# Kernel optimization log

Hardware: AMD Instinct MI355X
Metric: run time of the kernel (lower is better)

## Reference

```python
import jax, jax.numpy as jnp
from jax import lax
import numpy as np

T, B, I, U = 512, 64, 512, 512
FORGET_BIAS = 1.0  # matches forget_bias=1.0; cell_clip=None -> no clipping; no peephole


def setup_inputs() -> dict:
    key = jax.random.key(0)
    kx, kw = jax.random.split(key)
    x = jax.random.normal(kx, (T, B, I), dtype=jnp.float32)
    cs0 = jnp.zeros((B, U), dtype=jnp.float32)
    h0 = jnp.zeros((B, U), dtype=jnp.float32)
    # kernel [input_size + num_units, 4*num_units], bias [4*num_units] (zeros init as in build())
    w = jax.random.normal(kw, (I + U, 4 * U), dtype=jnp.float32) * 0.05
    b = jnp.zeros((4 * U,), dtype=jnp.float32)
    return {"x": x, "cs0": cs0, "h0": h0, "w": w, "b": b}


def reference(x, cs0, h0, w, b):
    """Fused BlockLSTM forward. Returns (h_seq [T,B,U], final_cs, final_h),
    mirroring LSTMBlockWrapper.call -> (outputs, (cell_state, output))."""

    def step(carry, x_t):
        cs_prev, h_prev = carry
        z = jnp.concatenate([x_t, h_prev], axis=-1) @ w + b  # [B, 4U]
        # TF BlockLSTM gate order: i, ci (cell input), f, o
        zi, zci, zf, zo = jnp.split(z, 4, axis=-1)
        i = jax.nn.sigmoid(zi)
        f = jax.nn.sigmoid(zf + FORGET_BIAS)
        ci = jnp.tanh(zci)
        cs = ci * i + cs_prev * f  # no cell_clip (cell_clip=-1)
        h = jnp.tanh(cs) * jax.nn.sigmoid(zo)
        return (cs, h), h

    (final_cs, final_h), h_seq = lax.scan(step, (cs0, h0), x)
    return h_seq, final_cs, final_h
```

## Files before the change

### kernel.cpp

```cpp
#include <hip/hip_runtime.h>


#define T_STEPS 512
#define NB 64
#define NU 512
#define NI 512
#define KTOT 1024
#define ZCOLS 2048
#define HSEQ_ELEMS (T_STEPS * NB * NU)
#define POISON64 0x7FC07FC07FC07FC0ull

typedef float    floatx4   __attribute__((ext_vector_type(4)));
typedef __bf16   bf16x8    __attribute__((ext_vector_type(8)));
typedef unsigned short ushortx8 __attribute__((ext_vector_type(8)));
typedef unsigned long long ull_t;

static __device__ __forceinline__ unsigned short f2bf(float f) {
  unsigned int u = __builtin_bit_cast(unsigned int, f);
  u += 0x7fffu + ((u >> 16) & 1u);
  return (unsigned short)(u >> 16);
}
static __device__ __forceinline__ float bf2f(unsigned short h) {
  unsigned int u = ((unsigned int)h) << 16;
  return __builtin_bit_cast(float, u);
}
static __device__ __forceinline__ float asf(unsigned int u) {
  return __builtin_bit_cast(float, u);
}
static __device__ __forceinline__ float sigmoidf_(float x) {
  return __builtin_amdgcn_rcpf(1.0f + __expf(-x));
}
static __device__ __forceinline__ float fast_tanhf(float x) {
  const float ax = fabsf(x);
  const float t = __expf(-2.0f * ax);
  const float r = (1.0f - t) * __builtin_amdgcn_rcpf(1.0f + t);
  return copysignf(r, x);
}
static __device__ __forceinline__ bf16x8 ldfrag(const unsigned short* p) {
  ushortx8 v = *reinterpret_cast<const ushortx8*>(p);
  return __builtin_bit_cast(bf16x8, v);
}
static __device__ __forceinline__ ull_t pack4bf(float a, float b, float c, float d) {
  return (ull_t)f2bf(a) | ((ull_t)f2bf(b) << 16) | ((ull_t)f2bf(c) << 32) |
         ((ull_t)f2bf(d) << 48);
}
static __device__ __forceinline__ bf16x8 mkfrag(ull_t lo, ull_t hi) {
  struct P { ull_t a, b; } s{lo, hi};
  return __builtin_bit_cast(bf16x8, s);
}

__global__ __launch_bounds__(256) void init_kernel(const float* __restrict__ h0,
                                                   unsigned short* __restrict__ hbf) {
  const int j = blockIdx.x * 256 + threadIdx.x;
  if (j < 524288) {
    ull_t* p = reinterpret_cast<ull_t*>(&hbf[32768 + (size_t)j * 32]);
#pragma unroll
    for (int r = 0; r < 8; ++r) p[r] = POISON64;
  } else {
    const int k = j - 524288;
#pragma unroll
    for (int p2 = 0; p2 < 2; ++p2) {
      const int i = k * 2 + p2;
      const int row = i >> 6, chunk = i & 63;
      const float* src = &h0[row * NU + chunk * 8];
      const ull_t lo = pack4bf(src[0], src[1], src[2], src[3]);
      const ull_t hi = pack4bf(src[4], src[5], src[6], src[7]);
      const size_t off = ((size_t)((row >> 5) * 64 + chunk) * 32 + (row & 31)) * 8;
      *reinterpret_cast<ull_t*>(&hbf[off]) = lo;
      *reinterpret_cast<ull_t*>(&hbf[off + 4]) = hi;
    }
  }
}

__global__ __launch_bounds__(256) void transpose_w_kernel(
    const float* __restrict__ w, unsigned short* __restrict__ wT) {
  __shared__ float tile[32][33];
  const int u0 = blockIdx.x * 32;
  const int k0 = blockIdx.y * 32;
  const int g = blockIdx.z;
  const int tx = threadIdx.x & 31, ty = threadIdx.x >> 5;
#pragma unroll
  for (int r = 0; r < 4; ++r) {
    const int k = ty + r * 8;
    tile[k][tx] = w[(size_t)(k0 + k) * ZCOLS + g * 512 + u0 + tx];
  }
  __syncthreads();
#pragma unroll
  for (int r = 0; r < 4; ++r) {
    const int u = ty + r * 8;
    wT[(size_t)((u0 + u) * 4 + g) * KTOT + k0 + tx] = f2bf(tile[tx][u]);
  }
}

__global__ __launch_bounds__(256) void gemm_zx_kernel(
    const float* __restrict__ x, const unsigned short* __restrict__ wT,
    const float* __restrict__ bias, unsigned short* __restrict__ zxp) {
  __shared__ __align__(16) unsigned short As[128][32];
  __shared__ __align__(16) unsigned short Bs[128][32];
  const int m0 = blockIdx.y * 128;
  const int n0 = blockIdx.x * 128;
  const int tid = threadIdx.x;
  const int wid = tid >> 6, lane = tid & 63;
  const int quad = lane >> 4, nl = lane & 15;
  const int wm = (wid & 1) * 64, wn = (wid >> 1) * 64;
  const int srow = tid >> 3;
  const int skk = (tid & 7) * 4;

  floatx4 acc[4][4] = {};

  for (int kt = 0; kt < 16; ++kt) {
    const int k0 = kt * 32;
    __syncthreads();
#pragma unroll
    for (int r = 0; r < 4; ++r) {
      const int row = r * 32 + srow;
      const float4 v =
          *reinterpret_cast<const float4*>(&x[(size_t)(m0 + row) * NI + k0 + skk]);
      *reinterpret_cast<ull_t*>(&As[row][skk]) = pack4bf(v.x, v.y, v.z, v.w);
      *reinterpret_cast<ull_t*>(&Bs[row][skk]) =
          *reinterpret_cast<const ull_t*>(&wT[(size_t)(n0 + row) * KTOT + k0 + skk]);
    }
    __syncthreads();
    bf16x8 af[4], bfr[4];
#pragma unroll
    for (int i = 0; i < 4; ++i) {
      af[i] = ldfrag(&As[wm + i * 16 + nl][quad * 8]);
      bfr[i] = ldfrag(&Bs[wn + i * 16 + nl][quad * 8]);
    }
#pragma unroll
    for (int i = 0; i < 4; ++i)
#pragma unroll
      for (int j = 0; j < 4; ++j)
        acc[i][j] =
            __builtin_amdgcn_mfma_f32_16x16x32_bf16(af[i], bfr[j], acc[i][j], 0, 0, 0);
  }

  float bv[4];
#pragma unroll
  for (int j = 0; j < 4; ++j) {
    const int colp = n0 + wn + j * 16 + nl;
    bv[j] = bias[(colp & 3) * 512 + (colp >> 2)];
  }
#pragma unroll
  for (int i = 0; i < 4; ++i) {
    const int browb = wm + i * 16 + quad * 4;
    const int t = (m0 + browb) >> 6;
    const int rt = (browb >> 5) & 1;
    const int hi = (browb & 31) >> 3;
    const int qb = (browb >> 2) & 1;
#pragma unroll
    for (int j = 0; j < 4; ++j) {
      const int colp = n0 + wn + j * 16 + nl;
      const int cbl = colp >> 5;
      const int lanep = (colp & 31) + 32 * qb;
      const ull_t packed =
          pack4bf(acc[i][j][0] + bv[j], acc[i][j][1] + bv[j],
                  acc[i][j][2] + bv[j], acc[i][j][3] + bv[j]);
      *reinterpret_cast<ull_t*>(
          &zxp[((((size_t)t * 64 + cbl) * 2 + rt) * 64 + lanep) * 16 + hi * 4]) = packed;
    }
  }
}

__global__ __launch_bounds__(64, 1) void lstm_rec_kernel(
    const unsigned short* __restrict__ zxp, const unsigned short* __restrict__ wT,
    const float* __restrict__ cs_init, float* __restrict__ out,
    unsigned short* __restrict__ hbf) {
  const int lane = threadIdx.x;
  const int bid = blockIdx.x;
  const int cb = bid >> 2;
  const int qr = bid & 3;
  const int l15 = lane & 15, lq = lane >> 4;
  const int u0 = cb * 8;
  const int rowg = qr * 16 + l15;
  const int rh = qr >> 1;
  const int r31 = (qr & 1) * 16 + l15;

  bf16x8 Bf[2][16];
#pragma unroll
  for (int cf = 0; cf < 2; ++cf)
#pragma unroll
    for (int kf = 0; kf < 16; ++kf)
      Bf[cf][kf] = ldfrag(
          &wT[(size_t)(cb * 32 + cf * 16 + l15) * KTOT + 512 + kf * 32 + lq * 8]);

  float csv[2];
  csv[0] = cs_init[rowg * NU + u0 + 2 * lq];
  csv[1] = cs_init[rowg * NU + u0 + 2 * lq + 1];

  __shared__ float zsh[2][16][33];

  ull_t AL[16], AH[16];
  const unsigned short* hpbase =
      hbf + (size_t)rh * 16384 + (size_t)r31 * 8;

  auto issueA = [&](int t) {
    const unsigned short* hp = hpbase + (size_t)t * 32768 + lq * 256;
#pragma unroll
    for (int kf = 0; kf < 16; ++kf) {
      const unsigned short* p = hp + kf * 1024;
      AL[kf] = __hip_atomic_load((const ull_t*)p, __ATOMIC_RELAXED,
                                 __HIP_MEMORY_SCOPE_AGENT);
      AH[kf] = __hip_atomic_load((const ull_t*)(p + 4), __ATOMIC_RELAXED,
                                 __HIP_MEMORY_SCOPE_AGENT);
    }
  };

  const int hi4 = (qr & 1) * 2 + (lq >> 1);
  const int lanep_base = l15 + 32 * (lq & 1);
  ull_t zx0, zx1;
  auto issueZ = [&](int t) {
    const size_t base = ((((size_t)t * 64 + cb) * 2 + rh) * 64);
    zx0 = *reinterpret_cast<const ull_t*>(
        &zxp[(base + lanep_base) * 16 + 4 * hi4]);
    zx1 = *reinterpret_cast<const ull_t*>(
        &zxp[(base + lanep_base + 16) * 16 + 4 * hi4]);
  };

  issueA(0);
  issueZ(0);

  for (int t = 0; t < T_STEPS; ++t) {
    {
      int guard = 0;
      while (true) {
        float sx = 0.f, sy = 0.f, sz = 0.f, sw = 0.f;
#pragma unroll
        for (int kf = 0; kf < 16; ++kf) {
          sx += asf((unsigned)(AL[kf] & 0xffffffffu));
          sy += asf((unsigned)(AL[kf] >> 32));
          sz += asf((unsigned)(AH[kf] & 0xffffffffu));
          sw += asf((unsigned)(AH[kf] >> 32));
        }
        const float c = (sx + sy) + (sz + sw);
        if (!__any(c != c) || ++guard >= (1 << 18)) break;
        issueA(t);
      }
    }

    floatx4 a00, a01;
#pragma unroll
    for (int r = 0; r < 4; ++r) {
      a00[r] = bf2f((unsigned short)((zx0 >> (16 * r)) & 0xffffu));
      a01[r] = bf2f((unsigned short)((zx1 >> (16 * r)) & 0xffffu));
    }
    floatx4 a10 = {0.f, 0.f, 0.f, 0.f}, a11 = {0.f, 0.f, 0.f, 0.f};
#pragma unroll
    for (int kf = 0; kf < 8; ++kf) {
      const bf16x8 Alo = mkfrag(AL[kf], AH[kf]);
      const bf16x8 Ahi = mkfrag(AL[8 + kf], AH[8 + kf]);
      a00 = __builtin_amdgcn_mfma_f32_16x16x32_bf16(Alo, Bf[0][kf], a00, 0, 0, 0);
      a01 = __builtin_amdgcn_mfma_f32_16x16x32_bf16(Alo, Bf[1][kf], a01, 0, 0, 0);
      a10 = __builtin_amdgcn_mfma_f32_16x16x32_bf16(Ahi, Bf[0][8 + kf], a10, 0, 0, 0);
      a11 = __builtin_amdgcn_mfma_f32_16x16x32_bf16(Ahi, Bf[1][8 + kf], a11, 0, 0, 0);
    }
    const floatx4 zc0 = a00 + a10;
    const floatx4 zc1 = a01 + a11;

    const int pb = t & 1;
#pragma unroll
    for (int r = 0; r < 4; ++r) {
      zsh[pb][lq * 4 + r][l15] = zc0[r];
      zsh[pb][lq * 4 + r][16 + l15] = zc1[r];
    }
    const float4 g0 = *reinterpret_cast<const float4*>(&zsh[pb][l15][8 * lq]);
    const float4 g1 = *reinterpret_cast<const float4*>(&zsh[pb][l15][8 * lq + 4]);

    float hout[2];
    {
      const float iv = sigmoidf_(g0.x);
      const float civ = fast_tanhf(g0.y);
      const float fv = sigmoidf_(g0.z + 1.0f);
      const float ov = sigmoidf_(g0.w);
      csv[0] = civ * iv + csv[0] * fv;
      hout[0] = fast_tanhf(csv[0]) * ov;
    }
    {
      const float iv = sigmoidf_(g1.x);
      const float civ = fast_tanhf(g1.y);
      const float fv = sigmoidf_(g1.z + 1.0f);
      const float ov = sigmoidf_(g1.w);
      csv[1] = civ * iv + csv[1] * fv;
      hout[1] = fast_tanhf(csv[1]) * ov;
    }

    unsigned short* hw = &hbf[(size_t)(t + 1) * 32768 + (size_t)rh * 16384 +
                              cb * 256 + r31 * 8 + 2 * lq];
    const unsigned hv = (unsigned)f2bf(hout[0]) | ((unsigned)f2bf(hout[1]) << 16);
    __hip_atomic_store(reinterpret_cast<unsigned*>(hw), hv, __ATOMIC_RELAXED,
                       __HIP_MEMORY_SCOPE_AGENT);
    asm volatile("" ::: "memory");
    if (t + 1 < T_STEPS) {
      issueA(t + 1);
      issueZ(t + 1);
    }

    float* op = &out[((size_t)t * NB + rowg) * NU + u0 + 2 * lq];
    op[0] = hout[0];
    op[1] = hout[1];
    if (t == T_STEPS - 1) {
      float* cp = &out[HSEQ_ELEMS + (size_t)rowg * NU + u0 + 2 * lq];
      cp[0] = csv[0];
      cp[1] = csv[1];
      float* hp2 = &out[HSEQ_ELEMS + NB * NU + (size_t)rowg * NU + u0 + 2 * lq];
      hp2[0] = hout[0];
      hp2[1] = hout[1];
    }
  }
}

extern "C" void kernel_launch(void* const* d_in, const int* in_sizes, int n_in,
                              void* d_out, int out_size, void* d_ws, size_t ws_size,
                              hipStream_t stream) {
  const float* x = (const float*)d_in[0];
  const float* cs0 = (const float*)d_in[1];
  const float* h0 = (const float*)d_in[2];
  const float* w = (const float*)d_in[3];
  const float* bias = (const float*)d_in[4];
  float* out = (float*)d_out;

  char* ws = (char*)d_ws;
  unsigned short* wT = (unsigned short*)(ws);
  unsigned short* zxp = (unsigned short*)(ws + (size_t)(4 << 20));
  unsigned short* hbf = (unsigned short*)(ws + (size_t)(132 << 20));

  init_kernel<<<dim3(2056), 256, 0, stream>>>(h0, hbf);
  transpose_w_kernel<<<dim3(16, 32, 4), 256, 0, stream>>>(w, wT);
  gemm_zx_kernel<<<dim3(16, 256), 256, 0, stream>>>(x, wT, bias, zxp);
  lstm_rec_kernel<<<dim3(256), 64, 0, stream>>>(zxp, wT, cs0, out, hbf);
}
```

Baseline: 1.308 ms.

## Repartition recurrent LSTM kernel to 512 blocks with transposed MFMA and new h layout

Result: slower. 1.944 ms (+48.6%).

```diff
diff --git a/kernel.cpp b/kernel.cpp
--- a/kernel.cpp
+++ b/kernel.cpp
@@ -24,9 +24,6 @@
   unsigned int u = ((unsigned int)h) << 16;
   return __builtin_bit_cast(float, u);
 }
-static __device__ __forceinline__ float asf(unsigned int u) {
-  return __builtin_bit_cast(float, u);
-}
 static __device__ __forceinline__ float sigmoidf_(float x) {
   return __builtin_amdgcn_rcpf(1.0f + __expf(-x));
 }
@@ -44,9 +41,11 @@
   return (ull_t)f2bf(a) | ((ull_t)f2bf(b) << 16) | ((ull_t)f2bf(c) << 32) |
          ((ull_t)f2bf(d) << 48);
 }
-static __device__ __forceinline__ bf16x8 mkfrag(ull_t lo, ull_t hi) {
+static __device__ __forceinline__ floatx4 ld_agent16f(const unsigned short* p) {
+  ull_t lo = __hip_atomic_load((const ull_t*)p, __ATOMIC_RELAXED, __HIP_MEMORY_SCOPE_AGENT);
+  ull_t hi = __hip_atomic_load((const ull_t*)(p + 4), __ATOMIC_RELAXED, __HIP_MEMORY_SCOPE_AGENT);
   struct P { ull_t a, b; } s{lo, hi};
-  return __builtin_bit_cast(bf16x8, s);
+  return __builtin_bit_cast(floatx4, s);
 }
 
 __global__ __launch_bounds__(256) void init_kernel(const float* __restrict__ h0,
@@ -63,9 +62,10 @@
       const int i = k * 2 + p2;
       const int row = i >> 6, chunk = i & 63;
       const float* src = &h0[row * NU + chunk * 8];
-      const ull_t lo = pack4bf(src[0], src[1], src[2], src[3]);
-      const ull_t hi = pack4bf(src[4], src[5], src[6], src[7]);
-      const size_t off = ((size_t)((row >> 5) * 64 + chunk) * 32 + (row & 31)) * 8;
+      const ull_t lo = pack4bf(src[0], src[4], src[1], src[5]);
+      const ull_t hi = pack4bf(src[2], src[6], src[3], src[7]);
+      const size_t off =
+          (size_t)(row >> 3) * 4096 + (size_t)chunk * 64 + (size_t)(row & 7) * 8;
       *reinterpret_cast<ull_t*>(&hbf[off]) = lo;
       *reinterpret_cast<ull_t*>(&hbf[off + 4]) = hi;
     }
@@ -88,7 +88,13 @@
 #pragma unroll
   for (int r = 0; r < 4; ++r) {
     const int u = ty + r * 8;
-    wT[(size_t)((u0 + u) * 4 + g) * KTOT + k0 + tx] = f2bf(tile[tx][u]);
+    const int kk = k0 + tx;
+    int kd = kk;
+    if (kk >= 512) {
+      const int u3 = kk & 7;
+      kd = (kk & ~7) | (((u3 & 3) << 1) | (u3 >> 2));
+    }
+    wT[(size_t)((u0 + u) * 4 + g) * KTOT + kd] = f2bf(tile[tx][u]);
   }
 }
 
@@ -162,19 +168,17 @@
   }
 }
 
-__global__ __launch_bounds__(64, 1) void lstm_rec_kernel(
+__global__ __launch_bounds__(64) void lstm_rec_kernel(
     const unsigned short* __restrict__ zxp, const unsigned short* __restrict__ wT,
     const float* __restrict__ cs_init, float* __restrict__ out,
     unsigned short* __restrict__ hbf) {
   const int lane = threadIdx.x;
   const int bid = blockIdx.x;
-  const int cb = bid >> 2;
-  const int qr = bid & 3;
+  const int g = bid & 7;
+  const int cb = bid >> 3;
   const int l15 = lane & 15, lq = lane >> 4;
-  const int u0 = cb * 8;
-  const int rowg = qr * 16 + l15;
-  const int rh = qr >> 1;
-  const int r31 = (qr & 1) * 16 + l15;
+  const int r8 = l15 & 7;
+  const int rowg = g * 8 + r8;
 
   bf16x8 Bf[2][16];
 #pragma unroll
@@ -185,126 +189,135 @@
           &wT[(size_t)(cb * 32 + cf * 16 + l15) * KTOT + 512 + kf * 32 + lq * 8]);
 
   float csv[2];
-  csv[0] = cs_init[rowg * NU + u0 + 2 * lq];
-  csv[1] = cs_init[rowg * NU + u0 + 2 * lq + 1];
-
-  __shared__ float zsh[2][16][33];
-
-  ull_t AL[16], AH[16];
-  const unsigned short* hpbase =
-      hbf + (size_t)rh * 16384 + (size_t)r31 * 8;
-
-  auto issueA = [&](int t) {
-    const unsigned short* hp = hpbase + (size_t)t * 32768 + lq * 256;
+  csv[0] = cs_init[rowg * NU + cb * 8 + lq];
+  csv[1] = cs_init[rowg * NU + cb * 8 + 4 + lq];
+
+  floatx4 Af[16];
+  unsigned short zxv[8];
+
+  auto issueL = [&](int tt) {
+    const unsigned short* p0 =
+        hbf + (size_t)tt * 32768 + g * 4096 + lq * 64 + r8 * 8;
 #pragma unroll
     for (int kf = 0; kf < 16; ++kf) {
-      const unsigned short* p = hp + kf * 1024;
-      AL[kf] = __hip_atomic_load((const ull_t*)p, __ATOMIC_RELAXED,
-                                 __HIP_MEMORY_SCOPE_AGENT);
-      AH[kf] = __hip_atomic_load((const ull_t*)(p + 4), __ATOMIC_RELAXED,
-                                 __HIP_MEMORY_SCOPE_AGENT);
+      asm volatile("global_load_dwordx4 %0, %1, off sc0"
+                   : "=v"(Af[kf])
+                   : "v"(p0 + (size_t)kf * 256)
+                   : "memory");
     }
   };
-
-  const int hi4 = (qr & 1) * 2 + (lq >> 1);
-  const int lanep_base = l15 + 32 * (lq & 1);
-  ull_t zx0, zx1;
-  auto issueZ = [&](int t) {
-    const size_t base = ((((size_t)t * 64 + cb) * 2 + rh) * 64);
-    zx0 = *reinterpret_cast<const ull_t*>(
-        &zxp[(base + lanep_base) * 16 + 4 * hi4]);
-    zx1 = *reinterpret_cast<const ull_t*>(
-        &zxp[(base + lanep_base + 16) * 16 + 4 * hi4]);
+  auto issueM = [&](int tt) {
+    const unsigned short* p0 =
+        hbf + (size_t)tt * 32768 + g * 4096 + lq * 64 + r8 * 8;
+#pragma unroll
+    for (int kf = 0; kf < 16; ++kf) Af[kf] = ld_agent16f(p0 + (size_t)kf * 256);
   };
-
-  issueA(0);
+  const int rt_ = rowg >> 5;
+  const int qb_ = (rowg >> 2) & 1;
+  const int hi_ = (rowg & 31) >> 3;
+  const int rr_ = rowg & 3;
+  auto issueZ = [&](int tt) {
+    const size_t base = (((size_t)tt * 64 + cb) * 2 + rt_) * 64;
+#pragma unroll
+    for (int cf = 0; cf < 2; ++cf)
+#pragma unroll
+      for (int r = 0; r < 4; ++r) {
+        const int c5 = cf * 16 + lq * 4 + r;
+        zxv[cf * 4 + r] = zxp[(base + (size_t)(c5 + 32 * qb_)) * 16 + hi_ * 4 + rr_];
+      }
+  };
+
+  issueL(0);
   issueZ(0);
 
+  int mstreak = 0;
+  bool preferM = false;
+
   for (int t = 0; t < T_STEPS; ++t) {
-    {
-      int guard = 0;
-      while (true) {
-        float sx = 0.f, sy = 0.f, sz = 0.f, sw = 0.f;
-#pragma unroll
-        for (int kf = 0; kf < 16; ++kf) {
-          sx += asf((unsigned)(AL[kf] & 0xffffffffu));
-          sy += asf((unsigned)(AL[kf] >> 32));
-          sz += asf((unsigned)(AH[kf] & 0xffffffffu));
-          sw += asf((unsigned)(AH[kf] >> 32));
-        }
-        const float c = (sx + sy) + (sz + sw);
-        if (!__any(c != c) || ++guard >= (1 << 18)) break;
-        issueA(t);
+    bool usedM = false;
+    int tries = 0;
+    while (true) {
+      asm volatile("s_waitcnt vmcnt(0)" ::: "memory");
+      __builtin_amdgcn_sched_barrier(0);
+      floatx4 vs = Af[0];
+#pragma unroll
+      for (int kf = 1; kf < 16; ++kf) vs += Af[kf];
+      const float s = (vs[0] + vs[1]) + (vs[2] + vs[3]);
+      if (!__any(s != s)) break;
+      if (++tries >= (1 << 18)) break;
+      if (!preferM && tries < 4) {
+        issueL(t);
+      } else {
+        usedM = true;
+        issueM(t);
       }
     }
-
-    floatx4 a00, a01;
-#pragma unroll
-    for (int r = 0; r < 4; ++r) {
-      a00[r] = bf2f((unsigned short)((zx0 >> (16 * r)) & 0xffffu));
-      a01[r] = bf2f((unsigned short)((zx1 >> (16 * r)) & 0xffffu));
-    }
-    floatx4 a10 = {0.f, 0.f, 0.f, 0.f}, a11 = {0.f, 0.f, 0.f, 0.f};
+    if (usedM) {
+      if (++mstreak > 8) preferM = true;
+    } else {
+      mstreak = 0;
+    }
+
+    floatx4 p00 = {0.f, 0.f, 0.f, 0.f}, p01 = {0.f, 0.f, 0.f, 0.f};
+    floatx4 p10 = {0.f, 0.f, 0.f, 0.f}, p11 = {0.f, 0.f, 0.f, 0.f};
 #pragma unroll
     for (int kf = 0; kf < 8; ++kf) {
-      const bf16x8 Alo = mkfrag(AL[kf], AH[kf]);
-      const bf16x8 Ahi = mkfrag(AL[8 + kf], AH[8 + kf]);
-      a00 = __builtin_amdgcn_mfma_f32_16x16x32_bf16(Alo, Bf[0][kf], a00, 0, 0, 0);
-      a01 = __builtin_amdgcn_mfma_f32_16x16x32_bf16(Alo, Bf[1][kf], a01, 0, 0, 0);
-      a10 = __builtin_amdgcn_mfma_f32_16x16x32_bf16(Ahi, Bf[0][8 + kf], a10, 0, 0, 0);
-      a11 = __builtin_amdgcn_mfma_f32_16x16x32_bf16(Ahi, Bf[1][8 + kf], a11, 0, 0, 0);
-    }
-    const floatx4 zc0 = a00 + a10;
-    const floatx4 zc1 = a01 + a11;
-
-    const int pb = t & 1;
-#pragma unroll
-    for (int r = 0; r < 4; ++r) {
-      zsh[pb][lq * 4 + r][l15] = zc0[r];
-      zsh[pb][lq * 4 + r][16 + l15] = zc1[r];
-    }
-    const float4 g0 = *reinterpret_cast<const float4*>(&zsh[pb][l15][8 * lq]);
-    const float4 g1 = *reinterpret_cast<const float4*>(&zsh[pb][l15][8 * lq + 4]);
+      const bf16x8 hlo = __builtin_bit_cast(bf16x8, Af[kf]);
+      const bf16x8 hhi = __builtin_bit_cast(bf16x8, Af[8 + kf]);
+      p00 = __builtin_amdgcn_mfma_f32_16x16x32_bf16(Bf[0][kf], hlo, p00, 0, 0, 0);
+      p01 = __builtin_amdgcn_mfma_f32_16x16x32_bf16(Bf[1][kf], hlo, p01, 0, 0, 0);
+      p10 = __builtin_amdgcn_mfma_f32_16x16x32_bf16(Bf[0][8 + kf], hhi, p10, 0, 0, 0);
+      p11 = __builtin_amdgcn_mfma_f32_16x16x32_bf16(Bf[1][8 + kf], hhi, p11, 0, 0, 0);
+    }
+    const floatx4 z0 = p00 + p10;
+    const floatx4 z1 = p01 + p11;
 
     float hout[2];
     {
-      const float iv = sigmoidf_(g0.x);
-      const float civ = fast_tanhf(g0.y);
-      const float fv = sigmoidf_(g0.z + 1.0f);
-      const float ov = sigmoidf_(g0.w);
+      const float iv = sigmoidf_(z0[0] + bf2f(zxv[0]));
+      const float civ = fast_tanhf(z0[1] + bf2f(zxv[1]));
+      const float fv = sigmoidf_(z0[2] + bf2f(zxv[2]) + 1.0f);
+      const float ov = sigmoidf_(z0[3] + bf2f(zxv[3]));
       csv[0] = civ * iv + csv[0] * fv;
       hout[0] = fast_tanhf(csv[0]) * ov;
     }
     {
-      const float iv = sigmoidf_(g1.x);
-      const float civ = fast_tanhf(g1.y);
-      const float fv = sigmoidf_(g1.z + 1.0f);
-      const float ov = sigmoidf_(g1.w);
+      const float iv = sigmoidf_(z1[0] + bf2f(zxv[4]));
+      const float civ = fast_tanhf(z1[1] + bf2f(zxv[5]));
+      const float fv = sigmoidf_(z1[2] + bf2f(zxv[6]) + 1.0f);
+      const float ov = sigmoidf_(z1[3] + bf2f(zxv[7]));
       csv[1] = civ * iv + csv[1] * fv;
       hout[1] = fast_tanhf(csv[1]) * ov;
     }
 
-    unsigned short* hw = &hbf[(size_t)(t + 1) * 32768 + (size_t)rh * 16384 +
-                              cb * 256 + r31 * 8 + 2 * lq];
-    const unsigned hv = (unsigned)f2bf(hout[0]) | ((unsigned)f2bf(hout[1]) << 16);
-    __hip_atomic_store(reinterpret_cast<unsigned*>(hw), hv, __ATOMIC_RELAXED,
-                       __HIP_MEMORY_SCOPE_AGENT);
-    asm volatile("" ::: "memory");
+    const unsigned hv =
+        (unsigned)f2bf(hout[0]) | ((unsigned)f2bf(hout[1]) << 16);
+    unsigned short* hw = &hbf[(size_t)(t + 1) * 32768 + g * 4096 + cb * 64 +
+                              r8 * 8 + 2 * lq];
+    if (l15 < 8) {
+      *(volatile unsigned*)hw = hv;
+      __hip_atomic_store(reinterpret_cast<unsigned*>(hw), hv, __ATOMIC_RELAXED,
+                         __HIP_MEMORY_SCOPE_AGENT);
+    }
+
     if (t + 1 < T_STEPS) {
-      issueA(t + 1);
+      if (!preferM) issueL(t + 1);
+      else          issueM(t + 1);
       issueZ(t + 1);
     }
 
-    float* op = &out[((size_t)t * NB + rowg) * NU + u0 + 2 * lq];
-    op[0] = hout[0];
-    op[1] = hout[1];
-    if (t == T_STEPS - 1) {
-      float* cp = &out[HSEQ_ELEMS + (size_t)rowg * NU + u0 + 2 * lq];
-      cp[0] = csv[0];
-      cp[1] = csv[1];
-      float* hp2 = &out[HSEQ_ELEMS + NB * NU + (size_t)rowg * NU + u0 + 2 * lq];
-      hp2[0] = hout[0];
-      hp2[1] = hout[1];
+    if (l15 < 8) {
+      float* op = &out[((size_t)t * NB + rowg) * NU + cb * 8];
+      op[lq] = hout[0];
+      op[4 + lq] = hout[1];
+      if (t == T_STEPS - 1) {
+        float* cp = &out[HSEQ_ELEMS + (size_t)rowg * NU + cb * 8];
+        cp[lq] = csv[0];
+        cp[4 + lq] = csv[1];
+        float* hp2 = &out[HSEQ_ELEMS + NB * NU + (size_t)rowg * NU + cb * 8];
+        hp2[lq] = hout[0];
+        hp2[4 + lq] = hout[1];
+      }
     }
   }
 }
@@ -327,5 +340,5 @@
   init_kernel<<<dim3(2056), 256, 0, stream>>>(h0, hbf);
   transpose_w_kernel<<<dim3(16, 32, 4), 256, 0, stream>>>(w, wT);
   gemm_zx_kernel<<<dim3(16, 256), 256, 0, stream>>>(x, wT, bias, zxp);
-  lstm_rec_kernel<<<dim3(256), 64, 0, stream>>>(zxp, wT, cs0, out, hbf);
-}
+  lstm_rec_kernel<<<dim3(512), 64, 0, stream>>>(zxp, wT, cs0, out, hbf);
+}
```
